# Kernel optimization log

Hardware: AMD Instinct MI355X
Metric: run time of the kernel (lower is better)

## Reference

```python
import jax, jax.numpy as jnp
import numpy as np
from jax import lax

H = W = 128
V = 16   # object_types
A = 8    # action_types
P = 64   # num_programs
C = 3    # input_channels
MAX_TIMEOUT = 50
DIRS = jnp.array([(1,0),(0,1),(-1,0),(0,-1),(1,1),(-1,1),(1,-1),(-1,-1)], dtype=jnp.int32)


def setup_inputs() -> dict:
    key = jax.random.key(0)
    ks = jax.random.split(key, 9)
    return {
        "obs": jax.random.normal(ks[0], (C, H, W), jnp.float32),
        "conv_w": jax.random.normal(ks[1], (V, C, 3, 3), jnp.float32) * 0.1,
        "conv_b": jax.random.normal(ks[2], (V,), jnp.float32) * 0.1,
        "w_obj": jax.random.normal(ks[3], (P, V), jnp.float32),
        "w_pos": jax.random.normal(ks[4], (P, V), jnp.float32),
        "w_neg": jax.random.normal(ks[5], (P, V), jnp.float32),
        "w_act": jax.random.normal(ks[6], (P, A), jnp.float32),
        "w_dir": jax.random.normal(ks[7], (P, 8), jnp.float32),
        "w_not": jax.random.normal(ks[8], (P, 2), jnp.float32),
    }


def reference(obs, conv_w, conv_b, w_obj, w_pos, w_neg, w_act, w_dir, w_not):
    # --- EntityExtractor: conv -> argmax over channels -> [H,W] object-id grid ---
    x = lax.conv_general_dilated(obs[None], conv_w, (1, 1), 'SAME',
                                 dimension_numbers=('NCHW', 'OIHW', 'NCHW'))
    grid = jnp.argmax(x[0] + conv_b[:, None, None], axis=0).astype(jnp.int32)  # [H,W]

    # first (row-major) occurrence of each object value, per at_cell_with_value/argwhere
    flat = grid.reshape(-1)                                   # [H*W]
    masks = flat[None, :] == jnp.arange(V, dtype=jnp.int32)[:, None]  # [V, H*W]
    exists = masks.any(axis=1)                                # [V]
    first = jnp.argmax(masks, axis=1).astype(jnp.int32)       # [V]
    fr, fc = first // W, first % W

    HW = H * W
    skey = jax.random.key(42)
    k1, k2, k3, k4, k5, k6 = jax.random.split(skey, 6)
    # one categorical sample per (cell, program) call, per-program logits
    def samp(k, logits):
        return jax.random.categorical(k, logits[None], shape=(HW, P)).reshape(-1)  # [N]
    s_obj = samp(k1, w_obj)
    s_pos = samp(k2, w_pos)
    s_neg = samp(k3, w_neg)
    s_act = samp(k4, w_act)
    s_dir = samp(k5, w_dir)
    s_not = samp(k6, w_not)

    r0 = fr[s_obj]                     # [N] start cell = first cell holding s_obj
    c0 = fc[s_obj]
    ex = exists[s_obj]                 # cell is None if object absent
    dr = DIRS[s_dir, 0]
    dc = DIRS[s_dir, 1]

    t = jnp.arange(1, MAX_TIMEOUT + 1, dtype=jnp.int32)       # [T]
    rs = r0[:, None] + t[None, :] * dr[:, None]               # [N,T]
    cs = c0[:, None] + t[None, :] * dc[:, None]
    inb = (rs >= 0) & (cs >= 0) & (rs < H) & (cs < W)
    vals = grid[jnp.clip(rs, 0, H - 1), jnp.clip(cs, 0, W - 1)]
    hit_pos = inb & (vals == s_pos[:, None])                  # true_condition
    stop = hit_pos | (inb & (vals == s_neg[:, None])) | ~inb  # any terminating event
    has = stop.any(axis=1)
    ft = jnp.argmax(stop, axis=1)                             # first event index
    cond = ex & has & jnp.take_along_axis(hit_pos, ft[:, None], axis=1)[:, 0]
    cond = cond ^ (s_not == 1)                                # is_not flip

    counts = jax.ops.segment_sum(cond.astype(jnp.float32), s_act, num_segments=A)
    return jax.nn.softmax(counts)
```

## Files before the change

### kernel.cpp

```cpp
#include <hip/hip_runtime.h>
#include <stdint.h>
#include <math.h>

#define Hh 128
#define Ww 128
#define Vn 16
#define An 8
#define Pn 64
#define Cn 3
#define HWc (Hh*Ww)
#define MAXT 50
#define NB 16
#define PB 64

__constant__ int c_DR[8] = {1, 0, -1, 0, 1, -1, 1, -1};
__constant__ int c_DC[8] = {0, 1, 0, -1, 1, 1, -1, -1};

__device__ __forceinline__ void softmaxS(const float* __restrict__ w,
                                         float* __restrict__ o, int n, int os) {
  float m = -INFINITY;
  for (int i = 0; i < n; ++i) m = fmaxf(m, w[i]);
  float s = 0.f;
  for (int i = 0; i < n; ++i) { float e = expf(w[i] - m); o[i * os] = e; s += e; }
  float inv = 1.f / s;
  for (int i = 0; i < n; ++i) o[i * os] *= inv;
}

__global__ __launch_bounds__(256) void k_prep(const float* __restrict__ obs,
                                              const float* __restrict__ cw,
                                              const float* __restrict__ cb,
                                              uint8_t* __restrict__ grid8,
                                              int* __restrict__ bf,
                                              uint32_t* __restrict__ done) {
  __shared__ float sw[Vn * Cn * 9];
  __shared__ float sb[Vn];
  __shared__ int lf[Vn];
  int t = threadIdx.x;
  for (int i = t; i < Vn * Cn * 9; i += 256) sw[i] = cw[i];
  if (t < Vn) { sb[t] = cb[t]; lf[t] = 0; }
  if (blockIdx.x == 0 && t == 0) *done = 0u;
  __syncthreads();

  int cell = blockIdx.x * 256 + t;
  int r = cell >> 7, c = cell & 127;
  float o[27];
#pragma unroll
  for (int ch = 0; ch < Cn; ++ch)
#pragma unroll
    for (int ky = 0; ky < 3; ++ky)
#pragma unroll
      for (int kx = 0; kx < 3; ++kx) {
        int rr = r + ky - 1, cc = c + kx - 1;
        o[ch * 9 + ky * 3 + kx] =
            ((unsigned)rr < (unsigned)Hh && (unsigned)cc < (unsigned)Ww)
                ? obs[(ch * Hh + rr) * Ww + cc] : 0.f;
      }
  float best = -INFINITY; int bi = 0;
#pragma unroll
  for (int v = 0; v < Vn; ++v) {
    float acc = sb[v];
#pragma unroll
    for (int i = 0; i < 27; ++i) acc += o[i] * sw[v * 27 + i];
    if (acc > best) { best = acc; bi = v; }
  }
  grid8[cell] = (uint8_t)bi;
  atomicMax(&lf[bi], HWc - cell);
  __syncthreads();
  if (t < Vn) bf[blockIdx.x * Vn + t] = lf[t];
}

__global__ __launch_bounds__(1024) void k_tail(const uint8_t* __restrict__ grid8g,
                                               const int* __restrict__ bf,
                                               const float* __restrict__ w_obj,
                                               const float* __restrict__ w_pos,
                                               const float* __restrict__ w_neg,
                                               const float* __restrict__ w_dir,
                                               const float* __restrict__ w_act,
                                               const float* __restrict__ w_not,
                                               float* __restrict__ qPart,
                                               uint32_t* __restrict__ done,
                                               float* __restrict__ out) {
  __shared__ uint8_t g8[HWc];
  __shared__ float2 sPPN[16 * 64];
  __shared__ float PObjT[16 * 64];
  __shared__ float PDirT[8 * 64];
  __shared__ float sAct[64 * 8];
  __shared__ float sNot[64 * 2];
  __shared__ uint32_t Ftab32[8 * 4];
  __shared__ uint32_t idxLo[8], idxHi[8], finM[8];
  __shared__ float qod[8 * 64];
  __shared__ int lf16[Vn], sEx[Vn], sFr[Vn], sFc[Vn];

  int t = threadIdx.x;
  int blk = blockIdx.x;
  int wave = t >> 6, lane = t & 63;

  ((uint4*)g8)[t] = ((const uint4*)grid8g)[t];
  if (t < Vn) lf16[t] = 0;
  __syncthreads();
  atomicMax(&lf16[t & 15], bf[t]);
  {
    int p = lane;
    if      (wave == 0) softmaxS(w_obj + p * 16, &PObjT[p], 16, 64);
    else if (wave == 1) softmaxS(w_pos + p * 16, &((float*)sPPN)[p * 2],     16, 128);
    else if (wave == 2) softmaxS(w_neg + p * 16, &((float*)sPPN)[p * 2 + 1], 16, 128);
    else if (wave == 3) softmaxS(w_dir + p * 8,  &PDirT[p], 8, 64);
    else if (wave == 4) softmaxS(w_act + p * 8,  &sAct[p * 8], 8, 1);
    else if (wave == 5) softmaxS(w_not + p * 2,  &sNot[p * 2], 2, 1);
  }
  __syncthreads();
  if (t < Vn) {
    int m = lf16[t];
    int ex = (m >= 1);
    sEx[t] = ex;
    int cell = ex ? (HWc - m) : 0;
    sFr[t] = cell >> 7;
    sFc[t] = cell & 127;
  }
  __syncthreads();

  if (wave < 8) {
    int so = blk, sd = wave;
    int step = lane + 1;
    int val = 255;
    if (step <= MAXT && sEx[so]) {
      int r = sFr[so] + step * c_DR[sd];
      int c = sFc[so] + step * c_DC[sd];
      if ((unsigned)r < (unsigned)Hh && (unsigned)c < (unsigned)Ww)
        val = g8[(r << 7) + c];
    }
    uint8_t* Fb = (uint8_t*)Ftab32;
#pragma unroll
    for (int v = 0; v < Vn; ++v) {
      unsigned long long m = __ballot(val == v);
      if (lane == v) Fb[wave * 16 + v] = m ? (uint8_t)__builtin_ctzll(m) : (uint8_t)64;
    }
  }
  __syncthreads();

  if (t < 8) {
    int F[16];
#pragma unroll
    for (int k = 0; k < 4; ++k) {
      uint32_t w = Ftab32[t * 4 + k];
#pragma unroll
      for (int b = 0; b < 4; ++b) F[k * 4 + b] = (w >> (8 * b)) & 0xFF;
    }
    uint32_t lo = 0, hi = 0, fm = 0;
#pragma unroll
    for (int v = 0; v < 16; ++v) {
      int rk = 0;
#pragma unroll
      for (int n = 0; n < 16; ++n)
        if (n != v) rk += (F[n] > F[v]) || (F[n] == F[v] && n < v);
      if (rk < 8) lo |= (uint32_t)v << (4 * rk);
      else        hi |= (uint32_t)v << (4 * (rk - 8));
      fm |= (F[v] < 64 ? 1u : 0u) << rk;
    }
    idxLo[t] = lo; idxHi[t] = hi; finM[t] = fm;
  }
  __syncthreads();

  if (wave < 8) {
    uint32_t lo = idxLo[wave], hi = idxHi[wave], fm = finM[wave];
    float acc = 0.f, inner = 0.f;
#pragma unroll
    for (int r = 0; r < 16; ++r) {
      uint32_t i = ((r < 8) ? (lo >> (4 * r)) : (hi >> (4 * (r - 8)))) & 15u;
      float2 pn = sPPN[i * 64 + lane];
      acc += pn.y;
      inner = fmaf(((fm >> r) & 1u) ? pn.x : 0.f, acc, inner);
    }
    qod[wave * 64 + lane] = PObjT[blk * 64 + lane] * PDirT[wave * 64 + lane] * inner;
  }
  __syncthreads();

  if (wave == 0) {
    float s = 0.f;
#pragma unroll
    for (int w = 0; w < 8; ++w) s += qod[w * 64 + lane];
    qPart[blk * 64 + lane] = s;

    __threadfence();
    uint32_t old = 0;
    if (lane == 0) old = atomicAdd(done, 1u);
    old = __shfl(old, 0, 64);
    if (old == (uint32_t)(NB - 1)) {
      __threadfence();
      float q = 0.f;
#pragma unroll
      for (int b = 0; b < NB; ++b)
        q += __hip_atomic_load(&qPart[b * 64 + lane],
                               __ATOMIC_RELAXED, __HIP_MEMORY_SCOPE_AGENT);
      float r = q * sNot[lane * 2] + (1.f - q) * sNot[lane * 2 + 1];
      float scale = 16384.f * r;
      float c[An];
#pragma unroll
      for (int a = 0; a < An; ++a) {
        float va = scale * sAct[lane * 8 + a];
#pragma unroll
        for (int off = 32; off >= 1; off >>= 1)
          va += __shfl_down(va, off, 64);
        c[a] = __shfl(va, 0, 64);
      }
      float m = -INFINITY;
#pragma unroll
      for (int a = 0; a < An; ++a) m = fmaxf(m, c[a]);
      float s2 = 0.f;
#pragma unroll
      for (int a = 0; a < An; ++a) s2 += expf(c[a] - m);
      if (lane < An) out[lane] = expf(c[lane] - m) / s2;
    }
  }
}

extern "C" void kernel_launch(void* const* d_in, const int* in_sizes, int n_in,
                              void* d_out, int out_size, void* d_ws, size_t ws_size,
                              hipStream_t stream) {
  const float* obs    = (const float*)d_in[0];
  const float* conv_w = (const float*)d_in[1];
  const float* conv_b = (const float*)d_in[2];
  const float* w_obj  = (const float*)d_in[3];
  const float* w_pos  = (const float*)d_in[4];
  const float* w_neg  = (const float*)d_in[5];
  const float* w_act  = (const float*)d_in[6];
  const float* w_dir  = (const float*)d_in[7];
  const float* w_not  = (const float*)d_in[8];
  float* out = (float*)d_out;

  uint8_t* ws = (uint8_t*)d_ws;
  int*      bf    = (int*)(ws + 0);
  uint8_t*  grid8 = ws + 4096;
  float*    qPart = (float*)(ws + 4096 + 16384);
  uint32_t* done  = (uint32_t*)(ws + 4096 + 16384 + 4096);

  k_prep<<<dim3(PB), dim3(256), 0, stream>>>(obs, conv_w, conv_b, grid8, bf, done);
  k_tail<<<dim3(NB), dim3(1024), 0, stream>>>(grid8, bf, w_obj, w_pos, w_neg,
                                              w_dir, w_act, w_not, qPart, done, out);
}
```

Measured before the change: 81.98 us.

## Fuse prep and tail kernels into one launch with inter-block flag sync

Merges the conv/argmax grid-building kernel and the per-object evaluation kernel into a single 64-block launch. Blocks publish completion through release-stored magic flags, and the first 16 blocks spin on those flags before reading the grid. A second flag array replaces the atomic counter for the final reduction. This removes one kernel launch and the gap between launches. The cost is spin-waiting, which relies on all blocks being co-resident. The stage-one flags are never reset, so on later calls the wait can pass on stale flags from the previous run.

```diff
diff --git a/kernel.cpp b/kernel.cpp
--- a/kernel.cpp
+++ b/kernel.cpp
@@ -11,7 +11,8 @@
 #define HWc (Hh*Ww)
 #define MAXT 50
 #define NB 16
-#define PB 64
+#define GB 64
+#define MAGIC 0x5EC0DE42u
 
 __constant__ int c_DR[8] = {1, 0, -1, 0, 1, -1, 1, -1};
 __constant__ int c_DC[8] = {0, 1, 0, -1, 1, 1, -1, -1};
@@ -26,60 +27,24 @@
   for (int i = 0; i < n; ++i) o[i * os] *= inv;
 }
 
-__global__ __launch_bounds__(256) void k_prep(const float* __restrict__ obs,
+__global__ __launch_bounds__(1024) void k_one(const float* __restrict__ obs,
                                               const float* __restrict__ cw,
                                               const float* __restrict__ cb,
+                                              const float* __restrict__ w_obj,
+                                              const float* __restrict__ w_pos,
+                                              const float* __restrict__ w_neg,
+                                              const float* __restrict__ w_dir,
+                                              const float* __restrict__ w_act,
+                                              const float* __restrict__ w_not,
                                               uint8_t* __restrict__ grid8,
                                               int* __restrict__ bf,
-                                              uint32_t* __restrict__ done) {
+                                              float* __restrict__ qPart,
+                                              uint32_t* __restrict__ flagA,
+                                              uint32_t* __restrict__ flagB,
+                                              float* __restrict__ out) {
   __shared__ float sw[Vn * Cn * 9];
   __shared__ float sb[Vn];
   __shared__ int lf[Vn];
-  int t = threadIdx.x;
-  for (int i = t; i < Vn * Cn * 9; i += 256) sw[i] = cw[i];
-  if (t < Vn) { sb[t] = cb[t]; lf[t] = 0; }
-  if (blockIdx.x == 0 && t == 0) *done = 0u;
-  __syncthreads();
-
-  int cell = blockIdx.x * 256 + t;
-  int r = cell >> 7, c = cell & 127;
-  float o[27];
-#pragma unroll
-  for (int ch = 0; ch < Cn; ++ch)
-#pragma unroll
-    for (int ky = 0; ky < 3; ++ky)
-#pragma unroll
-      for (int kx = 0; kx < 3; ++kx) {
-        int rr = r + ky - 1, cc = c + kx - 1;
-        o[ch * 9 + ky * 3 + kx] =
-            ((unsigned)rr < (unsigned)Hh && (unsigned)cc < (unsigned)Ww)
-                ? obs[(ch * Hh + rr) * Ww + cc] : 0.f;
-      }
-  float best = -INFINITY; int bi = 0;
-#pragma unroll
-  for (int v = 0; v < Vn; ++v) {
-    float acc = sb[v];
-#pragma unroll
-    for (int i = 0; i < 27; ++i) acc += o[i] * sw[v * 27 + i];
-    if (acc > best) { best = acc; bi = v; }
-  }
-  grid8[cell] = (uint8_t)bi;
-  atomicMax(&lf[bi], HWc - cell);
-  __syncthreads();
-  if (t < Vn) bf[blockIdx.x * Vn + t] = lf[t];
-}
-
-__global__ __launch_bounds__(1024) void k_tail(const uint8_t* __restrict__ grid8g,
-                                               const int* __restrict__ bf,
-                                               const float* __restrict__ w_obj,
-                                               const float* __restrict__ w_pos,
-                                               const float* __restrict__ w_neg,
-                                               const float* __restrict__ w_dir,
-                                               const float* __restrict__ w_act,
-                                               const float* __restrict__ w_not,
-                                               float* __restrict__ qPart,
-                                               uint32_t* __restrict__ done,
-                                               float* __restrict__ out) {
   __shared__ uint8_t g8[HWc];
   __shared__ float2 sPPN[16 * 64];
   __shared__ float PObjT[16 * 64];
@@ -95,10 +60,47 @@
   int blk = blockIdx.x;
   int wave = t >> 6, lane = t & 63;
 
-  ((uint4*)g8)[t] = ((const uint4*)grid8g)[t];
-  if (t < Vn) lf16[t] = 0;
-  __syncthreads();
-  atomicMax(&lf16[t & 15], bf[t]);
+  for (int i = t; i < Vn * Cn * 9; i += 1024) sw[i] = cw[i];
+  if (t < Vn) { sb[t] = cb[t]; lf[t] = 0; lf16[t] = 0; }
+  if (blk == GB - 1 && t < NB) flagB[t] = 0u;
+  __syncthreads();
+
+  if (t < 256) {
+    int cell = blk * 256 + t;
+    int r = cell >> 7, c = cell & 127;
+    float o[27];
+#pragma unroll
+    for (int ch = 0; ch < Cn; ++ch)
+#pragma unroll
+      for (int ky = 0; ky < 3; ++ky)
+#pragma unroll
+        for (int kx = 0; kx < 3; ++kx) {
+          int rr = r + ky - 1, cc = c + kx - 1;
+          o[ch * 9 + ky * 3 + kx] =
+              ((unsigned)rr < (unsigned)Hh && (unsigned)cc < (unsigned)Ww)
+                  ? obs[(ch * Hh + rr) * Ww + cc] : 0.f;
+        }
+    float best = -INFINITY; int bi = 0;
+#pragma unroll
+    for (int v = 0; v < Vn; ++v) {
+      float acc = sb[v];
+#pragma unroll
+      for (int i = 0; i < 27; ++i) acc += o[i] * sw[v * 27 + i];
+      if (acc > best) { best = acc; bi = v; }
+    }
+    grid8[cell] = (uint8_t)bi;
+    atomicMax(&lf[bi], HWc - cell);
+  }
+  __syncthreads();
+  if (t < Vn) bf[blk * Vn + t] = lf[t];
+  __syncthreads();
+  if (t == 0) {
+    __threadfence();
+    __hip_atomic_store(&flagA[blk], MAGIC, __ATOMIC_RELEASE,
+                       __HIP_MEMORY_SCOPE_AGENT);
+  }
+  if (blk >= NB) return;
+
   {
     int p = lane;
     if      (wave == 0) softmaxS(w_obj + p * 16, &PObjT[p], 16, 64);
@@ -108,6 +110,20 @@
     else if (wave == 4) softmaxS(w_act + p * 8,  &sAct[p * 8], 8, 1);
     else if (wave == 5) softmaxS(w_not + p * 2,  &sNot[p * 2], 2, 1);
   }
+
+  if (wave == 0) {
+    while (true) {
+      uint32_t v = __hip_atomic_load(&flagA[lane], __ATOMIC_ACQUIRE,
+                                     __HIP_MEMORY_SCOPE_AGENT);
+      if (__all(v == MAGIC)) break;
+      __builtin_amdgcn_s_sleep(8);
+    }
+  }
+  __syncthreads();
+  __threadfence();
+
+  ((uint4*)g8)[t] = ((const uint4*)grid8)[t];
+  atomicMax(&lf16[t & 15], bf[t]);
   __syncthreads();
   if (t < Vn) {
     int m = lf16[t];
@@ -180,12 +196,21 @@
 #pragma unroll
     for (int w = 0; w < 8; ++w) s += qod[w * 64 + lane];
     qPart[blk * 64 + lane] = s;
-
     __threadfence();
-    uint32_t old = 0;
-    if (lane == 0) old = atomicAdd(done, 1u);
-    old = __shfl(old, 0, 64);
-    if (old == (uint32_t)(NB - 1)) {
+
+    if (blk != 0) {
+      if (lane == 0)
+        __hip_atomic_store(&flagB[blk], MAGIC, __ATOMIC_RELEASE,
+                           __HIP_MEMORY_SCOPE_AGENT);
+    } else {
+      while (true) {
+        uint32_t v = (lane >= 1 && lane < NB)
+            ? __hip_atomic_load(&flagB[lane], __ATOMIC_ACQUIRE,
+                                __HIP_MEMORY_SCOPE_AGENT)
+            : MAGIC;
+        if (__all(v == MAGIC)) break;
+        __builtin_amdgcn_s_sleep(8);
+      }
       __threadfence();
       float q = 0.f;
 #pragma unroll
@@ -231,10 +256,12 @@
   uint8_t* ws = (uint8_t*)d_ws;
   int*      bf    = (int*)(ws + 0);
   uint8_t*  grid8 = ws + 4096;
-  float*    qPart = (float*)(ws + 4096 + 16384);
-  uint32_t* done  = (uint32_t*)(ws + 4096 + 16384 + 4096);
-
-  k_prep<<<dim3(PB), dim3(256), 0, stream>>>(obs, conv_w, conv_b, grid8, bf, done);
-  k_tail<<<dim3(NB), dim3(1024), 0, stream>>>(grid8, bf, w_obj, w_pos, w_neg,
-                                              w_dir, w_act, w_not, qPart, done, out);
+  float*    qPart = (float*)(ws + 20480);
+  uint32_t* flagA = (uint32_t*)(ws + 24576);
+  uint32_t* flagB = (uint32_t*)(ws + 24832);
+
+  k_one<<<dim3(GB), dim3(1024), 0, stream>>>(obs, conv_w, conv_b,
+                                             w_obj, w_pos, w_neg,
+                                             w_dir, w_act, w_not,
+                                             grid8, bf, qPart, flagA, flagB, out);
 }
```

Measured after the change: 85.73 us. 4.6% more time.
